# Kernel optimization log

Hardware: AMD Instinct MI355X
Metric: run time of the kernel (lower is better)

Reference implementation:

```python
import jax, jax.numpy as jnp
import numpy as np

N_HEADS = 8
TANH_CLIP = 10.0
NEG = -1e9  # finite stand-in for -inf so log_softmax/vjp stay NaN-free


def setup_inputs() -> dict:
    key = jax.random.key(0)
    ks = jax.random.split(key, 8)
    B, N, D = 256, 1000, 128
    embeddings = jax.random.normal(ks[0], (B, N, D), dtype=jnp.float32)
    W_node = jax.random.normal(ks[1], (D, 3 * D), dtype=jnp.float32) * (1.0 / np.sqrt(D))
    W_fixed = jax.random.normal(ks[2], (D, D), dtype=jnp.float32) * (1.0 / np.sqrt(D))
    W_step = jax.random.normal(ks[3], (2 * D, D), dtype=jnp.float32) * (1.0 / np.sqrt(2 * D))
    W_out = jax.random.normal(ks[4], (D, D), dtype=jnp.float32) * (1.0 / np.sqrt(D))
    first_idx = jax.random.randint(ks[5], (B,), 0, N)
    last_idx = jax.random.randint(ks[6], (B,), 0, N)
    mask = jax.random.randint(ks[7], (B, N), 0, 2).astype(jnp.bool_)
    mask = mask.at[:, 0].set(False)  # guarantee at least one feasible node
    return {"embeddings": embeddings, "W_node": W_node, "W_fixed": W_fixed,
            "W_step": W_step, "W_out": W_out, "first_idx": first_idx,
            "last_idx": last_idx, "mask": mask}


def reference(embeddings, W_node, W_fixed, W_step, W_out, first_idx, last_idx, mask):
    # One pointer-network decode step (TSP variant of AttentionModel._get_log_p),
    # including the _precompute projections.
    B, N, D = embeddings.shape
    H = N_HEADS
    dk = D // H

    # _precompute: fixed context + glimpse K/V + logit key
    graph_embed = embeddings.mean(axis=1)                       # [B, D]
    fixed_ctx = graph_embed @ W_fixed                           # [B, D]
    kvl = embeddings @ W_node                                   # [B, N, 3D]
    K, V, logit_K = jnp.split(kvl, 3, axis=-1)                  # each [B, N, D]

    # step context: cat(first-node emb, last-node emb) -> project to D
    b = jnp.arange(B)
    step_ctx = jnp.concatenate([embeddings[b, first_idx], embeddings[b, last_idx]], axis=-1)  # [B, 2D]
    q = fixed_ctx + step_ctx @ W_step                           # [B, D]

    # masked multi-head glimpse attention (q_len = 1)
    qh = q.reshape(B, H, dk)                                    # [B, H, dk]
    Kh = K.reshape(B, N, H, dk)
    Vh = V.reshape(B, N, H, dk)
    compat = jnp.einsum('bhd,bnhd->bhn', qh, Kh) / np.sqrt(dk)  # [B, H, N]
    compat = jnp.where(mask[:, None, :], NEG, compat)           # mask_inner
    attn = jax.nn.softmax(compat, axis=-1)
    heads = jnp.einsum('bhn,bnhd->bhd', attn, Vh)               # [B, H, dk]
    glimpse = heads.reshape(B, D) @ W_out                       # [B, D]

    # single-head logit attention with tanh clipping
    logits = jnp.einsum('bd,bnd->bn', glimpse, logit_K) / np.sqrt(D)  # [B, N]
    logits = jnp.tanh(logits) * TANH_CLIP
    logits = jnp.where(mask, NEG, logits)                       # mask_logits
    return jax.nn.log_softmax(logits, axis=-1)                  # [B, N]
```

## Files before the change

### kernel.cpp

```cpp
#include <hip/hip_runtime.h>


#define NEG (-1e9f)

__global__ __launch_bounds__(1024) void k_fused(
    const float* __restrict__ E, const float* __restrict__ Wn,
    const float* __restrict__ Wf, const float* __restrict__ Ws,
    const float* __restrict__ Wo,
    const int* __restrict__ fi, const int* __restrict__ li,
    const int* __restrict__ maskI, const unsigned char* __restrict__ maskB,
    float* __restrict__ out)
{
    const int b = blockIdx.x;
    const int t = threadIdx.x;

    __shared__ float4 Et[4096];
    __shared__ float4 qk4[256];
    __shared__ float4 pt4[256];
    __shared__ float4 EbarF4[256];
    __shared__ float4 mu4[32], e14[32], e24[32], gp4[32];
    __shared__ float q[128], heads[128], gl[128];
    __shared__ float qred[8][128];
    __shared__ float ct[128 * 9];
    __shared__ float redh[72];
    __shared__ float mh[8], lh[8], al[8];
    __shared__ float red[16];
    __shared__ float stat[2];
    __shared__ int flagS;

    float* const mu = (float*)mu4;
    float* const e1 = (float*)e14;
    float* const e2 = (float*)e24;
    float* const gp = (float*)gp4;
    float* const pt = (float*)pt4;
    float* const EbarF = (float*)EbarF4;
    float* const qkf = (float*)qk4;

    const float4* E4 = (const float4*)(E + (size_t)b * 128000);

    if (t == 0) flagS = 0;
    const uint4 dv = ((const uint4*)maskI)[t];
    const unsigned det = (dv.x | dv.y | dv.z | dv.w) & 0xFFFFFF00u;

    {
        const int cm = t & 31, sm = t >> 5;
        float4 acc = make_float4(0.f, 0.f, 0.f, 0.f);
        for (int r = sm; r < 1000; r += 32) {
            const float4 v = E4[r * 32 + cm];
            acc.x += v.x; acc.y += v.y; acc.z += v.z; acc.w += v.w;
        }
        Et[t] = acc;
    }
    if (t >= 512 && t < 544) {
        e14[t - 512] = E4[fi[b] * 32 + (t - 512)];
    } else if (t >= 544 && t < 576) {
        e24[t - 544] = E4[li[b] * 32 + (t - 544)];
    }
    __syncthreads();
    if (det) atomicOr(&flagS, 1);
    if (t < 32) {
        float4 acc = Et[t];
        #pragma unroll
        for (int s = 1; s < 32; ++s) {
            const float4 v = Et[s * 32 + t];
            acc.x += v.x; acc.y += v.y; acc.z += v.z; acc.w += v.w;
        }
        const float inv = 1.0f / 1000.0f;
        mu4[t] = make_float4(acc.x * inv, acc.y * inv, acc.z * inv, acc.w * inv);
    }
    __syncthreads();

    {
        const int part = t >> 7, d = t & 127;
        float acc = 0.f;
        const int k0 = part * 48;
        for (int k = k0; k < k0 + 48; ++k) {
            const float s = (k < 128) ? mu[k] : (k < 256 ? e1[k - 128] : e2[k - 256]);
            const float w = (k < 128) ? Wf[k * 128 + d] : Ws[(k - 128) * 128 + d];
            acc += s * w;
        }
        qred[part][d] = acc;
    }
    __syncthreads();
    if (t < 128) {
        float acc = 0.f;
        #pragma unroll
        for (int p = 0; p < 8; ++p) acc += qred[p][t];
        q[t] = acc;
    }
    __syncthreads();
    {
        const int j = t & 127, cg = t >> 7;
        const float qj = q[j];
        for (int c0 = 0; c0 < 128; c0 += 8) {
            const int c = c0 + cg;
            float v = Wn[c * 384 + j] * qj;
            v += __shfl_down(v, 8, 16);
            v += __shfl_down(v, 4, 16);
            v += __shfl_down(v, 2, 16);
            v += __shfl_down(v, 1, 16);
            if ((j & 15) == 0) {
                const int h = j >> 4, s = c >> 2;
                qkf[h * 128 + (s ^ (s >> 2)) * 4 + (c & 3)] = v * 0.25f;
            }
        }
    }
    __syncthreads();

    const bool useB = (flagS != 0);

    if (t < 8) { mh[t] = -3e38f; lh[t] = 0.f; }
    float4 eacc[8];
    #pragma unroll
    for (int h = 0; h < 8; ++h) eacc[h] = make_float4(0.f, 0.f, 0.f, 0.f);
    const int c4 = t & 31, sl = t >> 5;
    const int rr = t >> 3, qq = t & 7;

    for (int tile = 0; tile < 8; ++tile) {
        const int r0 = tile * 128;
        {
            const int g = r0 + rr;
            float4 v[4];
            if (g < 1000) {
                #pragma unroll
                for (int i = 0; i < 4; ++i) v[i] = E4[g * 32 + qq * 4 + i];
            } else {
                #pragma unroll
                for (int i = 0; i < 4; ++i) v[i] = make_float4(0.f, 0.f, 0.f, 0.f);
            }
            float pch[8];
            #pragma unroll
            for (int h = 0; h < 8; ++h) pch[h] = 0.f;
            #pragma unroll
            for (int i = 0; i < 4; ++i) {
                const int grp = qq * 4 + i;
                Et[rr * 32 + (grp ^ (rr & 7))] = v[i];
                const int sg = grp ^ (grp >> 2);
                #pragma unroll
                for (int h = 0; h < 8; ++h) {
                    const float4 w = qk4[h * 32 + sg];
                    pch[h] += v[i].x * w.x + v[i].y * w.y + v[i].z * w.z + v[i].w * w.w;
                }
            }
            #pragma unroll
            for (int m = 1; m <= 4; m <<= 1) {
                #pragma unroll
                for (int h = 0; h < 8; ++h) pch[h] += __shfl_xor(pch[h], m, 64);
            }
            bool msk = (g >= 1000);
            if (!msk) msk = useB ? (maskB[b * 1000 + g] != 0)
                                 : (maskI[b * 1000 + g] != 0);
            ct[rr * 9 + qq] = msk ? NEG : pch[qq];
        }
        __syncthreads();
        if (t < 64) {
            const int h = t & 7, part = t >> 3;
            float mt = -3e38f;
            const int rb = part * 16;
            for (int r = 0; r < 16; ++r) mt = fmaxf(mt, ct[(rb + r) * 9 + h]);
            redh[part * 9 + h] = mt;
        }
        __syncthreads();
        if (t < 8) {
            float mt = redh[t];
            for (int p = 1; p < 8; ++p) mt = fmaxf(mt, redh[p * 9 + t]);
            const float mnew = fmaxf(mh[t], mt);
            al[t] = __expf(mh[t] - mnew);
            mh[t] = mnew;
        }
        __syncthreads();
        {
            const int row = t >> 3, h = t & 7;
            pt[row * 8 + h] = __expf(ct[row * 9 + h] - mh[h]);
        }
        __syncthreads();
        {
            #pragma unroll
            for (int h = 0; h < 8; ++h) {
                const float a = al[h];
                eacc[h].x *= a; eacc[h].y *= a; eacc[h].z *= a; eacc[h].w *= a;
            }
            #pragma unroll
            for (int j = 0; j < 4; ++j) {
                const int r = sl * 4 + j;
                const float4 ev = Et[r * 32 + (c4 ^ (r & 7))];
                const float4 p0 = pt4[r * 2];
                const float4 p1 = pt4[r * 2 + 1];
                eacc[0].x += p0.x * ev.x; eacc[0].y += p0.x * ev.y; eacc[0].z += p0.x * ev.z; eacc[0].w += p0.x * ev.w;
                eacc[1].x += p0.y * ev.x; eacc[1].y += p0.y * ev.y; eacc[1].z += p0.y * ev.z; eacc[1].w += p0.y * ev.w;
                eacc[2].x += p0.z * ev.x; eacc[2].y += p0.z * ev.y; eacc[2].z += p0.z * ev.z; eacc[2].w += p0.z * ev.w;
                eacc[3].x += p0.w * ev.x; eacc[3].y += p0.w * ev.y; eacc[3].z += p0.w * ev.z; eacc[3].w += p0.w * ev.w;
                eacc[4].x += p1.x * ev.x; eacc[4].y += p1.x * ev.y; eacc[4].z += p1.x * ev.z; eacc[4].w += p1.x * ev.w;
                eacc[5].x += p1.y * ev.x; eacc[5].y += p1.y * ev.y; eacc[5].z += p1.y * ev.z; eacc[5].w += p1.y * ev.w;
                eacc[6].x += p1.z * ev.x; eacc[6].y += p1.z * ev.y; eacc[6].z += p1.z * ev.z; eacc[6].w += p1.z * ev.w;
                eacc[7].x += p1.w * ev.x; eacc[7].y += p1.w * ev.y; eacc[7].z += p1.w * ev.z; eacc[7].w += p1.w * ev.w;
            }
        }
        if (t < 64) {
            const int h = t & 7, part = t >> 3;
            float s = 0.f;
            const int rb = part * 16;
            for (int r = 0; r < 16; ++r) s += pt[(rb + r) * 8 + h];
            redh[part * 9 + h] = s;
        }
        __syncthreads();
        if (t < 8) {
            float s = 0.f;
            for (int p = 0; p < 8; ++p) s += redh[p * 9 + t];
            lh[t] = lh[t] * al[t] + s;
        }
    }

    if (sl >= 16) {
        #pragma unroll
        for (int h = 0; h < 8; ++h) Et[(sl - 16) * 256 + h * 32 + c4] = eacc[h];
    }
    __syncthreads();
    if (sl < 16) {
        #pragma unroll
        for (int h = 0; h < 8; ++h) {
            const float4 o = Et[sl * 256 + h * 32 + c4];
            eacc[h].x += o.x; eacc[h].y += o.y; eacc[h].z += o.z; eacc[h].w += o.w;
            Et[sl * 256 + h * 32 + c4] = eacc[h];
        }
    }
    __syncthreads();
    if (t < 256) {
        const int h = t >> 5, cc = t & 31;
        float4 s = make_float4(0.f, 0.f, 0.f, 0.f);
        #pragma unroll
        for (int s2 = 0; s2 < 16; ++s2) {
            const float4 v = Et[s2 * 256 + h * 32 + cc];
            s.x += v.x; s.y += v.y; s.z += v.z; s.w += v.w;
        }
        const float invl = 1.0f / lh[h];
        EbarF4[h * 32 + cc] = make_float4(s.x * invl, s.y * invl, s.z * invl, s.w * invl);
    }
    __syncthreads();

    {
        const int part = t >> 7, d = t & 127, h = d >> 4;
        float acc = 0.f;
        const int c0 = part * 16;
        for (int c = c0; c < c0 + 16; ++c) acc += EbarF[h * 128 + c] * Wn[c * 384 + 128 + d];
        qred[part][d] = acc;
    }
    __syncthreads();
    if (t < 128) {
        float acc = 0.f;
        #pragma unroll
        for (int p = 0; p < 8; ++p) acc += qred[p][t];
        heads[t] = acc;
    }
    __syncthreads();
    {
        const int part = t >> 7, d = t & 127;
        float acc = 0.f;
        const int j0 = part * 16;
        for (int j = j0; j < j0 + 16; ++j) acc += heads[j] * Wo[j * 128 + d];
        qred[part][d] = acc;
    }
    __syncthreads();
    if (t < 128) {
        float acc = 0.f;
        #pragma unroll
        for (int p = 0; p < 8; ++p) acc += qred[p][t];
        gl[t] = acc;
    }
    __syncthreads();
    {
        const int part = t >> 7, c = t & 127;
        float acc = 0.f;
        const int d0 = part * 16;
        for (int d = d0; d < d0 + 16; ++d) acc += Wn[c * 384 + 256 + d] * gl[d];
        qred[part][c] = acc;
    }
    __syncthreads();
    if (t < 128) {
        float acc = 0.f;
        #pragma unroll
        for (int p = 0; p < 8; ++p) acc += qred[p][t];
        gp[t] = acc * 0.08838834764831845f;
    }
    __syncthreads();

    {
        const int row = t >> 3, sub = t & 7;
        for (int tile = 0; tile < 8; ++tile) {
            const int g = tile * 128 + row;
            float acc = 0.f;
            if (g < 1000) {
                #pragma unroll
                for (int i = 0; i < 4; ++i) {
                    const float4 v = E4[g * 32 + sub * 4 + i];
                    const float4 w = gp4[sub * 4 + i];
                    acc += v.x * w.x + v.y * w.y + v.z * w.z + v.w * w.w;
                }
            }
            ct[row * 9 + sub] = acc;
            __syncthreads();
            if (t < 128) {
                const int g2 = tile * 128 + t;
                if (g2 < 1000) {
                    float s = 0.f;
                    #pragma unroll
                    for (int k = 0; k < 8; ++k) s += ct[t * 9 + k];
                    float zz = 10.0f * tanhf(s);
                    const bool m = useB ? (maskB[b * 1000 + g2] != 0)
                                        : (maskI[b * 1000 + g2] != 0);
                    if (m) zz = NEG;
                    pt[g2] = zz;
                }
            }
            __syncthreads();
        }
    }
    float v = (t < 1000) ? pt[t] : -3e38f;
    #pragma unroll
    for (int off = 32; off > 0; off >>= 1) v = fmaxf(v, __shfl_down(v, off, 64));
    if ((t & 63) == 0) red[t >> 6] = v;
    __syncthreads();
    if (t == 0) {
        float m = red[0];
        for (int i = 1; i < 16; ++i) m = fmaxf(m, red[i]);
        stat[0] = m;
    }
    __syncthreads();
    float sv = (t < 1000) ? __expf(pt[t] - stat[0]) : 0.f;
    #pragma unroll
    for (int off = 32; off > 0; off >>= 1) sv += __shfl_down(sv, off, 64);
    if ((t & 63) == 0) red[t >> 6] = sv;
    __syncthreads();
    if (t == 0) {
        float s = 0.f;
        for (int i = 0; i < 16; ++i) s += red[i];
        stat[1] = stat[0] + __logf(s);
    }
    __syncthreads();
    if (t < 1000)
        out[(size_t)b * 1000 + t] = pt[t] - stat[1];
}

extern "C" void kernel_launch(void* const* d_in, const int* in_sizes, int n_in,
                              void* d_out, int out_size, void* d_ws, size_t ws_size,
                              hipStream_t stream) {
    const float* E  = (const float*)d_in[0];
    const float* Wn = (const float*)d_in[1];
    const float* Wf = (const float*)d_in[2];
    const float* Ws = (const float*)d_in[3];
    const float* Wo = (const float*)d_in[4];
    const int*   fi = (const int*)d_in[5];
    const int*   li = (const int*)d_in[6];
    const int*   maskI = (const int*)d_in[7];
    const unsigned char* maskB = (const unsigned char*)d_in[7];
    float* out = (float*)d_out;

    k_fused<<<256, 1024, 0, stream>>>(E, Wn, Wf, Ws, Wo, fi, li, maskI, maskB, out);
}
```

Before: 284.4 us.

## Drop online-softmax max tracking, prefetch next tile, use fixed bounds for log-softmax

```diff
diff --git a/kernel.cpp b/kernel.cpp
--- a/kernel.cpp
+++ b/kernel.cpp
@@ -14,27 +14,26 @@
     const int b = blockIdx.x;
     const int t = threadIdx.x;
 
-    __shared__ float4 Et[4096];
+    __shared__ float4 Et4[4096];
     __shared__ float4 qk4[256];
     __shared__ float4 pt4[256];
-    __shared__ float4 EbarF4[256];
     __shared__ float4 mu4[32], e14[32], e24[32], gp4[32];
+    __shared__ float EbarF[1024];
     __shared__ float q[128], heads[128], gl[128];
     __shared__ float qred[8][128];
-    __shared__ float ct[128 * 9];
-    __shared__ float redh[72];
-    __shared__ float mh[8], lh[8], al[8];
+    __shared__ float redh[144];
+    __shared__ float linv[8];
     __shared__ float red[16];
-    __shared__ float stat[2];
+    __shared__ float stat[1];
     __shared__ int flagS;
 
-    float* const mu = (float*)mu4;
-    float* const e1 = (float*)e14;
-    float* const e2 = (float*)e24;
-    float* const gp = (float*)gp4;
-    float* const pt = (float*)pt4;
-    float* const EbarF = (float*)EbarF4;
+    float* const mu  = (float*)mu4;
+    float* const e1  = (float*)e14;
+    float* const e2  = (float*)e24;
+    float* const gp  = (float*)gp4;
+    float* const pt  = (float*)pt4;
     float* const qkf = (float*)qk4;
+    float* const Etf = (float*)Et4;
 
     const float4* E4 = (const float4*)(E + (size_t)b * 128000);
 
@@ -49,7 +48,7 @@
             const float4 v = E4[r * 32 + cm];
             acc.x += v.x; acc.y += v.y; acc.z += v.z; acc.w += v.w;
         }
-        Et[t] = acc;
+        Et4[t] = acc;
     }
     if (t >= 512 && t < 544) {
         e14[t - 512] = E4[fi[b] * 32 + (t - 512)];
@@ -59,10 +58,10 @@
     __syncthreads();
     if (det) atomicOr(&flagS, 1);
     if (t < 32) {
-        float4 acc = Et[t];
+        float4 acc = Et4[t];
         #pragma unroll
         for (int s = 1; s < 32; ++s) {
-            const float4 v = Et[s * 32 + t];
+            const float4 v = Et4[s * 32 + t];
             acc.x += v.x; acc.y += v.y; acc.z += v.z; acc.w += v.w;
         }
         const float inv = 1.0f / 1000.0f;
@@ -89,152 +88,116 @@
         q[t] = acc;
     }
     __syncthreads();
+
+    const int rr = t >> 3, qq = t & 7;
+    float4 v[4];
+    #pragma unroll
+    for (int i = 0; i < 4; ++i) v[i] = E4[rr * 32 + qq * 4 + i];
+    int miC = maskI[b * 1000 + rr];
+    unsigned char mbC = maskB[b * 1000 + rr];
+
     {
         const int j = t & 127, cg = t >> 7;
         const float qj = q[j];
         for (int c0 = 0; c0 < 128; c0 += 8) {
             const int c = c0 + cg;
-            float v = Wn[c * 384 + j] * qj;
-            v += __shfl_down(v, 8, 16);
-            v += __shfl_down(v, 4, 16);
-            v += __shfl_down(v, 2, 16);
-            v += __shfl_down(v, 1, 16);
+            float vv = Wn[c * 384 + j] * qj;
+            vv += __shfl_down(vv, 8, 16);
+            vv += __shfl_down(vv, 4, 16);
+            vv += __shfl_down(vv, 2, 16);
+            vv += __shfl_down(vv, 1, 16);
             if ((j & 15) == 0) {
                 const int h = j >> 4, s = c >> 2;
-                qkf[h * 128 + (s ^ (s >> 2)) * 4 + (c & 3)] = v * 0.25f;
-            }
-        }
-    }
-    __syncthreads();
-
+                qkf[h * 128 + (s ^ (s >> 2)) * 4 + (c & 3)] = vv * 0.25f;
+            }
+        }
+    }
+    __syncthreads();
     const bool useB = (flagS != 0);
 
-    if (t < 8) { mh[t] = -3e38f; lh[t] = 0.f; }
-    float4 eacc[8];
+    const int esl = t >> 7, ec = t & 127;
+    float eacc[8];
     #pragma unroll
-    for (int h = 0; h < 8; ++h) eacc[h] = make_float4(0.f, 0.f, 0.f, 0.f);
-    const int c4 = t & 31, sl = t >> 5;
-    const int rr = t >> 3, qq = t & 7;
+    for (int h = 0; h < 8; ++h) eacc[h] = 0.f;
+    float lacc = 0.f;
 
     for (int tile = 0; tile < 8; ++tile) {
-        const int r0 = tile * 128;
-        {
-            const int g = r0 + rr;
-            float4 v[4];
-            if (g < 1000) {
-                #pragma unroll
-                for (int i = 0; i < 4; ++i) v[i] = E4[g * 32 + qq * 4 + i];
-            } else {
-                #pragma unroll
-                for (int i = 0; i < 4; ++i) v[i] = make_float4(0.f, 0.f, 0.f, 0.f);
-            }
-            float pch[8];
-            #pragma unroll
-            for (int h = 0; h < 8; ++h) pch[h] = 0.f;
-            #pragma unroll
-            for (int i = 0; i < 4; ++i) {
-                const int grp = qq * 4 + i;
-                Et[rr * 32 + (grp ^ (rr & 7))] = v[i];
-                const int sg = grp ^ (grp >> 2);
-                #pragma unroll
-                for (int h = 0; h < 8; ++h) {
-                    const float4 w = qk4[h * 32 + sg];
-                    pch[h] += v[i].x * w.x + v[i].y * w.y + v[i].z * w.z + v[i].w * w.w;
-                }
-            }
-            #pragma unroll
-            for (int m = 1; m <= 4; m <<= 1) {
-                #pragma unroll
-                for (int h = 0; h < 8; ++h) pch[h] += __shfl_xor(pch[h], m, 64);
-            }
-            bool msk = (g >= 1000);
-            if (!msk) msk = useB ? (maskB[b * 1000 + g] != 0)
-                                 : (maskI[b * 1000 + g] != 0);
-            ct[rr * 9 + qq] = msk ? NEG : pch[qq];
-        }
-        __syncthreads();
-        if (t < 64) {
-            const int h = t & 7, part = t >> 3;
-            float mt = -3e38f;
-            const int rb = part * 16;
-            for (int r = 0; r < 16; ++r) mt = fmaxf(mt, ct[(rb + r) * 9 + h]);
-            redh[part * 9 + h] = mt;
-        }
-        __syncthreads();
-        if (t < 8) {
-            float mt = redh[t];
-            for (int p = 1; p < 8; ++p) mt = fmaxf(mt, redh[p * 9 + t]);
-            const float mnew = fmaxf(mh[t], mt);
-            al[t] = __expf(mh[t] - mnew);
-            mh[t] = mnew;
-        }
-        __syncthreads();
-        {
-            const int row = t >> 3, h = t & 7;
-            pt[row * 8 + h] = __expf(ct[row * 9 + h] - mh[h]);
-        }
-        __syncthreads();
-        {
+        const int lr = tile * 128 + rr;
+        const bool valid = (lr < 1000);
+        float pch[8];
+        #pragma unroll
+        for (int h = 0; h < 8; ++h) pch[h] = 0.f;
+        #pragma unroll
+        for (int i = 0; i < 4; ++i) {
+            const int grp = qq * 4 + i;
+            Et4[rr * 32 + grp] = v[i];
+            const int sg = grp ^ (grp >> 2);
             #pragma unroll
             for (int h = 0; h < 8; ++h) {
-                const float a = al[h];
-                eacc[h].x *= a; eacc[h].y *= a; eacc[h].z *= a; eacc[h].w *= a;
-            }
+                const float4 w = qk4[h * 32 + sg];
+                pch[h] += v[i].x * w.x + v[i].y * w.y + v[i].z * w.z + v[i].w * w.w;
+            }
+        }
+        #pragma unroll
+        for (int m = 1; m <= 4; m <<= 1) {
             #pragma unroll
-            for (int j = 0; j < 4; ++j) {
-                const int r = sl * 4 + j;
-                const float4 ev = Et[r * 32 + (c4 ^ (r & 7))];
-                const float4 p0 = pt4[r * 2];
-                const float4 p1 = pt4[r * 2 + 1];
-                eacc[0].x += p0.x * ev.x; eacc[0].y += p0.x * ev.y; eacc[0].z += p0.x * ev.z; eacc[0].w += p0.x * ev.w;
-                eacc[1].x += p0.y * ev.x; eacc[1].y += p0.y * ev.y; eacc[1].z += p0.y * ev.z; eacc[1].w += p0.y * ev.w;
-                eacc[2].x += p0.z * ev.x; eacc[2].y += p0.z * ev.y; eacc[2].z += p0.z * ev.z; eacc[2].w += p0.z * ev.w;
-                eacc[3].x += p0.w * ev.x; eacc[3].y += p0.w * ev.y; eacc[3].z += p0.w * ev.z; eacc[3].w += p0.w * ev.w;
-                eacc[4].x += p1.x * ev.x; eacc[4].y += p1.x * ev.y; eacc[4].z += p1.x * ev.z; eacc[4].w += p1.x * ev.w;
-                eacc[5].x += p1.y * ev.x; eacc[5].y += p1.y * ev.y; eacc[5].z += p1.y * ev.z; eacc[5].w += p1.y * ev.w;
-                eacc[6].x += p1.z * ev.x; eacc[6].y += p1.z * ev.y; eacc[6].z += p1.z * ev.z; eacc[6].w += p1.z * ev.w;
-                eacc[7].x += p1.w * ev.x; eacc[7].y += p1.w * ev.y; eacc[7].z += p1.w * ev.z; eacc[7].w += p1.w * ev.w;
-            }
-        }
-        if (t < 64) {
+            for (int h = 0; h < 8; ++h) pch[h] += __shfl_xor(pch[h], m, 8);
+        }
+        const bool msk = !valid || (useB ? (mbC != 0) : (miC != 0));
+        pt[rr * 8 + qq] = msk ? 0.f : __expf(pch[qq]);
+
+        float4 vn[4];
+        int miN = 1; unsigned char mbN = 1;
+        #pragma unroll
+        for (int i = 0; i < 4; ++i) vn[i] = make_float4(0.f, 0.f, 0.f, 0.f);
+        if (tile < 7) {
+            const int lr2 = lr + 128;
+            if (lr2 < 1000) {
+                #pragma unroll
+                for (int i = 0; i < 4; ++i) vn[i] = E4[lr2 * 32 + qq * 4 + i];
+                miN = maskI[b * 1000 + lr2];
+                mbN = maskB[b * 1000 + lr2];
+            }
+        }
+        __syncthreads();
+        #pragma unroll
+        for (int j = 0; j < 16; ++j) {
+            const int r = esl * 16 + j;
+            const float ev = Etf[r * 128 + ec];
+            const float4 p0 = pt4[r * 2];
+            const float4 p1 = pt4[r * 2 + 1];
+            eacc[0] += p0.x * ev; eacc[1] += p0.y * ev;
+            eacc[2] += p0.z * ev; eacc[3] += p0.w * ev;
+            eacc[4] += p1.x * ev; eacc[5] += p1.y * ev;
+            eacc[6] += p1.z * ev; eacc[7] += p1.w * ev;
+        }
+        if (t < 128) {
             const int h = t & 7, part = t >> 3;
-            float s = 0.f;
-            const int rb = part * 16;
-            for (int r = 0; r < 16; ++r) s += pt[(rb + r) * 8 + h];
-            redh[part * 9 + h] = s;
+            #pragma unroll
+            for (int r = 0; r < 8; ++r) lacc += pt[(part * 8 + r) * 8 + h];
         }
         __syncthreads();
-        if (t < 8) {
-            float s = 0.f;
-            for (int p = 0; p < 8; ++p) s += redh[p * 9 + t];
-            lh[t] = lh[t] * al[t] + s;
-        }
-    }
-
-    if (sl >= 16) {
-        #pragma unroll
-        for (int h = 0; h < 8; ++h) Et[(sl - 16) * 256 + h * 32 + c4] = eacc[h];
-    }
-    __syncthreads();
-    if (sl < 16) {
-        #pragma unroll
-        for (int h = 0; h < 8; ++h) {
-            const float4 o = Et[sl * 256 + h * 32 + c4];
-            eacc[h].x += o.x; eacc[h].y += o.y; eacc[h].z += o.z; eacc[h].w += o.w;
-            Et[sl * 256 + h * 32 + c4] = eacc[h];
-        }
-    }
-    __syncthreads();
-    if (t < 256) {
-        const int h = t >> 5, cc = t & 31;
-        float4 s = make_float4(0.f, 0.f, 0.f, 0.f);
-        #pragma unroll
-        for (int s2 = 0; s2 < 16; ++s2) {
-            const float4 v = Et[s2 * 256 + h * 32 + cc];
-            s.x += v.x; s.y += v.y; s.z += v.z; s.w += v.w;
-        }
-        const float invl = 1.0f / lh[h];
-        EbarF4[h * 32 + cc] = make_float4(s.x * invl, s.y * invl, s.z * invl, s.w * invl);
+        #pragma unroll
+        for (int i = 0; i < 4; ++i) v[i] = vn[i];
+        miC = miN; mbC = mbN;
+    }
+
+    #pragma unroll
+    for (int h = 0; h < 8; ++h) Etf[esl * 1024 + h * 128 + ec] = eacc[h];
+    if (t < 128) redh[(t >> 3) * 9 + (t & 7)] = lacc;
+    __syncthreads();
+    if (t < 8) {
+        float s = 0.f;
+        #pragma unroll
+        for (int p = 0; p < 16; ++p) s += redh[p * 9 + t];
+        linv[t] = 1.0f / s;
+    }
+    __syncthreads();
+    {
+        float s = 0.f;
+        #pragma unroll
+        for (int sl = 0; sl < 8; ++sl) s += Etf[sl * 1024 + t];
+        EbarF[t] = s * linv[t >> 7];
     }
     __syncthreads();
 
@@ -285,60 +248,46 @@
     __syncthreads();
 
     {
-        const int row = t >> 3, sub = t & 7;
         for (int tile = 0; tile < 8; ++tile) {
-            const int g = tile * 128 + row;
+            const int lr = tile * 128 + rr;
             float acc = 0.f;
-            if (g < 1000) {
+            if (lr < 1000) {
                 #pragma unroll
                 for (int i = 0; i < 4; ++i) {
-                    const float4 v = E4[g * 32 + sub * 4 + i];
-                    const float4 w = gp4[sub * 4 + i];
-                    acc += v.x * w.x + v.y * w.y + v.z * w.z + v.w * w.w;
+                    const float4 vv = E4[lr * 32 + qq * 4 + i];
+                    const float4 ww = gp4[qq * 4 + i];
+                    acc += vv.x * ww.x + vv.y * ww.y + vv.z * ww.z + vv.w * ww.w;
                 }
             }
-            ct[row * 9 + sub] = acc;
-            __syncthreads();
-            if (t < 128) {
-                const int g2 = tile * 128 + t;
-                if (g2 < 1000) {
-                    float s = 0.f;
-                    #pragma unroll
-                    for (int k = 0; k < 8; ++k) s += ct[t * 9 + k];
-                    float zz = 10.0f * tanhf(s);
-                    const bool m = useB ? (maskB[b * 1000 + g2] != 0)
-                                        : (maskI[b * 1000 + g2] != 0);
-                    if (m) zz = NEG;
-                    pt[g2] = zz;
-                }
-            }
-            __syncthreads();
-        }
-    }
-    float v = (t < 1000) ? pt[t] : -3e38f;
-    #pragma unroll
-    for (int off = 32; off > 0; off >>= 1) v = fmaxf(v, __shfl_down(v, off, 64));
-    if ((t & 63) == 0) red[t >> 6] = v;
-    __syncthreads();
-    if (t == 0) {
-        float m = red[0];
-        for (int i = 1; i < 16; ++i) m = fmaxf(m, red[i]);
-        stat[0] = m;
-    }
-    __syncthreads();
-    float sv = (t < 1000) ? __expf(pt[t] - stat[0]) : 0.f;
-    #pragma unroll
-    for (int off = 32; off > 0; off >>= 1) sv += __shfl_down(sv, off, 64);
-    if ((t & 63) == 0) red[t >> 6] = sv;
+            acc += __shfl_xor(acc, 1, 8);
+            acc += __shfl_xor(acc, 2, 8);
+            acc += __shfl_xor(acc, 4, 8);
+            if (qq == 0 && lr < 1000) {
+                float zz = 10.0f * tanhf(acc);
+                const bool m = useB ? (maskB[b * 1000 + lr] != 0)
+                                    : (maskI[b * 1000 + lr] != 0);
+                if (m) zz = NEG;
+                pt[lr] = zz;
+            }
+        }
+    }
+    __syncthreads();
+    {
+        float sv = (t < 1000) ? __expf(pt[t] - 10.0f) : 0.f;
+        #pragma unroll
+        for (int off = 32; off > 0; off >>= 1) sv += __shfl_down(sv, off, 64);
+        if ((t & 63) == 0) red[t >> 6] = sv;
+    }
     __syncthreads();
     if (t == 0) {
         float s = 0.f;
+        #pragma unroll
         for (int i = 0; i < 16; ++i) s += red[i];
-        stat[1] = stat[0] + __logf(s);
+        stat[0] = 10.0f + __logf(s);
     }
     __syncthreads();
     if (t < 1000)
-        out[(size_t)b * 1000 + t] = pt[t] - stat[1];
+        out[(size_t)b * 1000 + t] = pt[t] - stat[0];
 }
 
 extern "C" void kernel_launch(void* const* d_in, const int* in_sizes, int n_in,
@@ -355,5 +304,6 @@
     const unsigned char* maskB = (const unsigned char*)d_in[7];
     float* out = (float*)d_out;
 
-    k_fused<<<256, 1024, 0, stream>>>(E, Wn, Wf, Ws, Wo, fi, li, maskI, maskB, out);
+    k_fused<<<dim3(256), dim3(1024), 0, stream>>>(
+        E, Wn, Wf, Ws, Wo, fi, li, maskI, maskB, out);
 }
```

Measured after the change: 568.7 us. 2x slower.
